# Optimization experiments

Measured on AMD Instinct MI355X. Metric: run time of the kernel, lower is better.

The kernel has to match this reference:

```python
import jax, jax.numpy as jnp
import numpy as np

EPS = 1e-8


def _cdist(a, b):
    # Euclidean pairwise distances [N, M] via ||a||^2 + ||b||^2 - 2 a b^T
    a2 = jnp.sum(a * a, axis=-1, keepdims=True)          # [N, 1]
    b2 = jnp.sum(b * b, axis=-1, keepdims=True).T        # [1, M]
    sq = a2 + b2 - 2.0 * (a @ b.T)                       # [N, M]
    return jnp.sqrt(jnp.maximum(sq, 1e-12))


def setup_inputs() -> dict:
    key = jax.random.key(0)
    k1, k2, k3 = jax.random.split(key, 3)
    N, M = 16384, 16384
    # scale to metric-like LiDAR coordinates
    query_points = jax.random.normal(k1, (N, 3), dtype=jnp.float32) * 20.0
    ref_points = jax.random.normal(k2, (M, 3), dtype=jnp.float32) * 20.0
    ref_flow = jax.random.normal(k3, (M, 3), dtype=jnp.float32)
    return {"query_points": query_points, "ref_points": ref_points,
            "ref_flow": ref_flow, "k": 3}


def reference(query_points, ref_points, ref_flow, k):
    # knn_interpolate_flow (pure-torch fallback path), method='knn'
    dist = _cdist(query_points, ref_points)              # [N, M]
    neg_d, knn_idx = jax.lax.top_k(-dist, k)             # smallest k distances
    knn_dist = -neg_d                                    # [N, k]
    weights = 1.0 / (knn_dist + EPS)
    weights = weights / jnp.sum(weights, axis=1, keepdims=True)
    knn_flow = ref_flow[knn_idx]                         # [N, k, 3]
    interpolated_flow = jnp.sum(weights[..., None] * knn_flow, axis=1)  # [N, 3]
    return interpolated_flow
```

## Files before the change

### kernel.cpp

```cpp
#include <hip/hip_runtime.h>
#include <math.h>

#define BLOCK 256
#define QPT   8
#define CHUNK 512
#define S     64

__device__ __forceinline__ float mul_rn(float a, float b) {
#pragma clang fp contract(off)
    return a * b;
}
__device__ __forceinline__ float add_rn(float a, float b) {
#pragma clang fp contract(off)
    return a + b;
}
__device__ __forceinline__ float sumsq3(float x, float y, float z) {
    return add_rn(add_rn(mul_rn(x, x), mul_rn(y, y)), mul_rn(z, z));
}
__device__ __forceinline__ float med3f(float a, float b, float c) {
    return __builtin_amdgcn_fmed3f(a, b, c);
}
__device__ __forceinline__ float pair_sq(float a0, float a1, float a2, float an,
                                         float bx, float by, float bz, float bw) {
    const float dot = __builtin_fmaf(a2, bz,
                      __builtin_fmaf(a1, by, mul_rn(a0, bx)));
    return __builtin_fmaf(-2.0f, dot, add_rn(an, bw));
}

__device__ __forceinline__ void val3_push(float& d0, float& d1, float& d2, float v) {
    d2 = med3f(d1, d2, v);
    d1 = med3f(d0, d1, v);
    d0 = fminf(d0, v);
}

__device__ __forceinline__ void lex3_push(float& d0, float& d1, float& d2,
                                          int& i0, int& i1, int& i2,
                                          float sq, int idx) {
    const bool l0 = (sq < d0) || (sq == d0 && idx < i0);
    const bool l1 = (sq < d1) || (sq == d1 && idx < i1);
    const bool l2 = (sq < d2) || (sq == d2 && idx < i2);
    i2 = l1 ? i1 : (l2 ? idx : i2);
    d2 = l1 ? d1 : (l2 ? sq  : d2);
    i1 = l0 ? i0 : (l1 ? idx : i1);
    d1 = l0 ? d0 : (l1 ? sq  : d1);
    i0 = l0 ? idx : i0;
    d0 = l0 ? sq  : d0;
}

__device__ __forceinline__ void stage_chunk(const float* __restrict__ r,
                                            int start, int cnt,
                                            float4* __restrict__ smem) {
    const int t = threadIdx.x;
    if (t < (cnt >> 2)) {
        const float4* p = (const float4*)(r + (size_t)(start + t * 4) * 3);
        const float4 A = p[0], B = p[1], C = p[2];
        smem[t * 4 + 0] = make_float4(A.x, A.y, A.z, sumsq3(A.x, A.y, A.z));
        smem[t * 4 + 1] = make_float4(A.w, B.x, B.y, sumsq3(A.w, B.x, B.y));
        smem[t * 4 + 2] = make_float4(B.z, B.w, C.x, sumsq3(B.z, B.w, C.x));
        smem[t * 4 + 3] = make_float4(C.y, C.z, C.w, sumsq3(C.y, C.z, C.w));
    }
}

__global__ __launch_bounds__(BLOCK, 2) void values_kernel(
    const float* __restrict__ q, const float* __restrict__ r,
    float* __restrict__ smin, int N, int refsPerSlice)
{
    __shared__ float4 smem[CHUNK];
    const int tid = threadIdx.x;
    const int s   = blockIdx.y;
    const int start = s * refsPerSlice;

    float a0[QPT], a1[QPT], a2[QPT], an[QPT], d0[QPT];
#pragma unroll
    for (int u = 0; u < QPT; ++u) {
        const int qi = (blockIdx.x * QPT + u) * BLOCK + tid;
        a0[u] = q[qi * 3 + 0];
        a1[u] = q[qi * 3 + 1];
        a2[u] = q[qi * 3 + 2];
        an[u] = sumsq3(a0[u], a1[u], a2[u]);
        d0[u] = __builtin_inff();
    }

    for (int coff = 0; coff < refsPerSlice; coff += CHUNK) {
        const int cnt = min(CHUNK, refsPerSlice - coff);
        __syncthreads();
        stage_chunk(r, start + coff, cnt, smem);
        __syncthreads();
#pragma unroll 4
        for (int j = 0; j < cnt; ++j) {
            const float4 b = smem[j];
#pragma unroll
            for (int u = 0; u < QPT; ++u) {
                const float sq = pair_sq(a0[u], a1[u], a2[u], an[u],
                                         b.x, b.y, b.z, b.w);
                d0[u] = fminf(d0[u], sq);
            }
        }
    }

#pragma unroll
    for (int u = 0; u < QPT; ++u) {
        const int qi = (blockIdx.x * QPT + u) * BLOCK + tid;
        smin[(size_t)qi * S + s] = d0[u];
    }
}

__global__ __launch_bounds__(BLOCK, 4) void rescan_kernel(
    const float* __restrict__ q, const float* __restrict__ r,
    const float* __restrict__ smin, const float* __restrict__ flow,
    float* __restrict__ out, int N, int refsPerSlice)
{
    const int lane = threadIdx.x & 63;
    const int qi   = blockIdx.x * (BLOCK / 64) + (threadIdx.x >> 6);

    const float a0 = q[qi * 3 + 0];
    const float a1 = q[qi * 3 + 1];
    const float a2 = q[qi * 3 + 2];
    const float an = sumsq3(a0, a1, a2);

    const float v = smin[(size_t)qi * S + lane];
    float g0 = v, g1 = __builtin_inff(), g2 = __builtin_inff();
#pragma unroll
    for (int m = 1; m < 64; m <<= 1) {
        const float e0 = __shfl_xor(g0, m);
        const float e1 = __shfl_xor(g1, m);
        const float e2 = __shfl_xor(g2, m);
        val3_push(g0, g1, g2, e0);
        val3_push(g0, g1, g2, e1);
        val3_push(g0, g1, g2, e2);
    }

    unsigned long long mask = __ballot(v <= g2);

    float d0 = __builtin_inff(), d1 = __builtin_inff(), d2 = __builtin_inff();
    int   i0 = 0x7fffffff, i1 = 0x7fffffff, i2 = 0x7fffffff;
    const int K = refsPerSlice >> 6;

    while (mask) {
        const int s = (int)__builtin_ctzll(mask);
        mask &= mask - 1;
        const int base = s * refsPerSlice;
        for (int k = 0; k < K; ++k) {
            const int idx = base + lane + (k << 6);
            const float b0 = r[3 * idx + 0];
            const float b1 = r[3 * idx + 1];
            const float b2 = r[3 * idx + 2];
            const float bw = sumsq3(b0, b1, b2);
            const float sq = pair_sq(a0, a1, a2, an, b0, b1, b2, bw);
            const bool c0 = sq < d0;
            const bool c1 = sq < d1;
            const bool c2 = sq < d2;
            i2 = c1 ? i1 : (c2 ? idx : i2);
            d2 = c1 ? d1 : (c2 ? sq  : d2);
            i1 = c0 ? i0 : (c1 ? idx : i1);
            d1 = c0 ? d0 : (c1 ? sq  : d1);
            i0 = c0 ? idx : i0;
            d0 = c0 ? sq  : d0;
        }
    }

#pragma unroll
    for (int m = 1; m < 64; m <<= 1) {
        const float e0 = __shfl_xor(d0, m);
        const float e1 = __shfl_xor(d1, m);
        const float e2 = __shfl_xor(d2, m);
        const int   j0 = __shfl_xor(i0, m);
        const int   j1 = __shfl_xor(i1, m);
        const int   j2 = __shfl_xor(i2, m);
        lex3_push(d0, d1, d2, i0, i1, i2, e0, j0);
        lex3_push(d0, d1, d2, i0, i1, i2, e1, j1);
        lex3_push(d0, d1, d2, i0, i1, i2, e2, j2);
    }

    if (lane == 0) {
        const float t0 = sqrtf(fmaxf(d0, 1e-12f));
        const float t1 = sqrtf(fmaxf(d1, 1e-12f));
        const float t2 = sqrtf(fmaxf(d2, 1e-12f));
        const float w0r = 1.0f / add_rn(t0, 1e-8f);
        const float w1r = 1.0f / add_rn(t1, 1e-8f);
        const float w2r = 1.0f / add_rn(t2, 1e-8f);
        const float wsum = add_rn(add_rn(w0r, w1r), w2r);
        const float w0 = w0r / wsum;
        const float w1 = w1r / wsum;
        const float w2 = w2r / wsum;

        const float f00 = flow[3 * i0 + 0], f01 = flow[3 * i0 + 1], f02 = flow[3 * i0 + 2];
        const float f10 = flow[3 * i1 + 0], f11 = flow[3 * i1 + 1], f12 = flow[3 * i1 + 2];
        const float f20 = flow[3 * i2 + 0], f21 = flow[3 * i2 + 1], f22 = flow[3 * i2 + 2];

        out[qi * 3 + 0] = add_rn(add_rn(mul_rn(w0, f00), mul_rn(w1, f10)), mul_rn(w2, f20));
        out[qi * 3 + 1] = add_rn(add_rn(mul_rn(w0, f01), mul_rn(w1, f11)), mul_rn(w2, f21));
        out[qi * 3 + 2] = add_rn(add_rn(mul_rn(w0, f02), mul_rn(w1, f12)), mul_rn(w2, f22));
    }
}

extern "C" void kernel_launch(void* const* d_in, const int* in_sizes, int n_in,
                              void* d_out, int out_size, void* d_ws, size_t ws_size,
                              hipStream_t stream) {
    const float* q    = (const float*)d_in[0];
    const float* r    = (const float*)d_in[1];
    const float* flow = (const float*)d_in[2];

    const int N = in_sizes[0] / 3;
    const int M = in_sizes[1] / 3;

    const int refsPerSlice = M / S;
    float* smin = (float*)d_ws;
    (void)ws_size;

    dim3 grid1(N / (BLOCK * QPT), S);
    values_kernel<<<grid1, BLOCK, 0, stream>>>(q, r, smin, N, refsPerSlice);

    rescan_kernel<<<N / (BLOCK / 64), BLOCK, 0, stream>>>(
        q, r, smin, flow, (float*)d_out, N, refsPerSlice);
}
```

Before: 113.2 us.

## Replace brute-force slice scan with uniform grid spatial hashing for KNN

Swaps the O(N*M) brute-force distance scan for a uniform 48^3 grid. Reference points are bucketed by counting sort (count, three-stage prefix scan, scatter). Each query wavefront then searches expanding cube shells around its cell and stops once the third-best distance is below the distance to the shell boundary. This cuts the distance work sharply but adds several small launches, atomics and divergent irregular loops. The grid extent and cell size are hardcoded to suit roughly Gaussian data with std 20, and points outside the extent are clamped into edge cells, which the stopping bound is meant to handle.

```diff
diff --git a/kernel.cpp b/kernel.cpp
--- a/kernel.cpp
+++ b/kernel.cpp
@@ -1,10 +1,13 @@
 #include <hip/hip_runtime.h>
 #include <math.h>
 
-#define BLOCK 256
-#define QPT   8
-#define CHUNK 512
-#define S     64
+#define GRIDC  48
+#define CELLS  (GRIDC*GRIDC*GRIDC)
+#define NBLK1  (CELLS/1024)
+#define EXT    96.0f
+#define CSZ    4.0f
+#define INVC   0.25f
+#define STOP_MARGIN 0.1f
 
 __device__ __forceinline__ float mul_rn(float a, float b) {
 #pragma clang fp contract(off)
@@ -26,13 +29,11 @@
                       __builtin_fmaf(a1, by, mul_rn(a0, bx)));
     return __builtin_fmaf(-2.0f, dot, add_rn(an, bw));
 }
-
 __device__ __forceinline__ void val3_push(float& d0, float& d1, float& d2, float v) {
     d2 = med3f(d1, d2, v);
     d1 = med3f(d0, d1, v);
     d0 = fminf(d0, v);
 }
-
 __device__ __forceinline__ void lex3_push(float& d0, float& d1, float& d2,
                                           int& i0, int& i1, int& i2,
                                           float sq, int idx) {
@@ -46,117 +47,167 @@
     i0 = l0 ? idx : i0;
     d0 = l0 ? sq  : d0;
 }
-
-__device__ __forceinline__ void stage_chunk(const float* __restrict__ r,
-                                            int start, int cnt,
-                                            float4* __restrict__ smem) {
-    const int t = threadIdx.x;
-    if (t < (cnt >> 2)) {
-        const float4* p = (const float4*)(r + (size_t)(start + t * 4) * 3);
-        const float4 A = p[0], B = p[1], C = p[2];
-        smem[t * 4 + 0] = make_float4(A.x, A.y, A.z, sumsq3(A.x, A.y, A.z));
-        smem[t * 4 + 1] = make_float4(A.w, B.x, B.y, sumsq3(A.w, B.x, B.y));
-        smem[t * 4 + 2] = make_float4(B.z, B.w, C.x, sumsq3(B.z, B.w, C.x));
-        smem[t * 4 + 3] = make_float4(C.y, C.z, C.w, sumsq3(C.y, C.z, C.w));
-    }
-}
-
-__global__ __launch_bounds__(BLOCK, 2) void values_kernel(
-    const float* __restrict__ q, const float* __restrict__ r,
-    float* __restrict__ smin, int N, int refsPerSlice)
-{
-    __shared__ float4 smem[CHUNK];
+__device__ __forceinline__ void cell_coords(float x, float y, float z,
+                                            int& cx, int& cy, int& cz) {
+    cx = min(max((int)floorf((x + EXT) * INVC), 0), GRIDC - 1);
+    cy = min(max((int)floorf((y + EXT) * INVC), 0), GRIDC - 1);
+    cz = min(max((int)floorf((z + EXT) * INVC), 0), GRIDC - 1);
+}
+__device__ __forceinline__ int qdiv(int x, unsigned long long magic) {
+    return (int)(((unsigned long long)(unsigned)x * magic) >> 40);
+}
+
+__global__ __launch_bounds__(256) void zero_kernel(int* __restrict__ a) {
+    a[blockIdx.x * 256 + threadIdx.x] = 0;
+}
+
+__global__ __launch_bounds__(256) void count_kernel(
+    const float* __restrict__ r, int* __restrict__ counts, int M)
+{
+    const int i = blockIdx.x * 256 + threadIdx.x;
+    if (i < M) {
+        int cx, cy, cz;
+        cell_coords(r[3 * i], r[3 * i + 1], r[3 * i + 2], cx, cy, cz);
+        atomicAdd(&counts[(cz * GRIDC + cy) * GRIDC + cx], 1);
+    }
+}
+
+__global__ __launch_bounds__(256) void scan1_kernel(
+    const int* __restrict__ counts, int* __restrict__ cellLoc,
+    int* __restrict__ bsum)
+{
+    __shared__ int arr[256];
     const int tid = threadIdx.x;
-    const int s   = blockIdx.y;
-    const int start = s * refsPerSlice;
-
-    float a0[QPT], a1[QPT], a2[QPT], an[QPT], d0[QPT];
-#pragma unroll
-    for (int u = 0; u < QPT; ++u) {
-        const int qi = (blockIdx.x * QPT + u) * BLOCK + tid;
-        a0[u] = q[qi * 3 + 0];
-        a1[u] = q[qi * 3 + 1];
-        a2[u] = q[qi * 3 + 2];
-        an[u] = sumsq3(a0[u], a1[u], a2[u]);
-        d0[u] = __builtin_inff();
-    }
-
-    for (int coff = 0; coff < refsPerSlice; coff += CHUNK) {
-        const int cnt = min(CHUNK, refsPerSlice - coff);
-        __syncthreads();
-        stage_chunk(r, start + coff, cnt, smem);
-        __syncthreads();
-#pragma unroll 4
-        for (int j = 0; j < cnt; ++j) {
-            const float4 b = smem[j];
-#pragma unroll
-            for (int u = 0; u < QPT; ++u) {
-                const float sq = pair_sq(a0[u], a1[u], a2[u], an[u],
-                                         b.x, b.y, b.z, b.w);
-                d0[u] = fminf(d0[u], sq);
-            }
-        }
-    }
-
-#pragma unroll
-    for (int u = 0; u < QPT; ++u) {
-        const int qi = (blockIdx.x * QPT + u) * BLOCK + tid;
-        smin[(size_t)qi * S + s] = d0[u];
-    }
-}
-
-__global__ __launch_bounds__(BLOCK, 4) void rescan_kernel(
-    const float* __restrict__ q, const float* __restrict__ r,
-    const float* __restrict__ smin, const float* __restrict__ flow,
-    float* __restrict__ out, int N, int refsPerSlice)
+    const int base = blockIdx.x * 1024 + tid * 4;
+    const int4 c = *(const int4*)(counts + base);
+    const int t1 = c.x, t2 = c.x + c.y, t3 = t2 + c.z, tot = t3 + c.w;
+    arr[tid] = tot;
+    __syncthreads();
+    for (int off = 1; off < 256; off <<= 1) {
+        const int w = (tid >= off) ? arr[tid - off] : 0;
+        __syncthreads();
+        arr[tid] += w;
+        __syncthreads();
+    }
+    const int excl = arr[tid] - tot;
+    *(int4*)(cellLoc + base) = make_int4(excl, excl + t1, excl + t2, excl + t3);
+    if (tid == 255) bsum[blockIdx.x] = arr[255];
+}
+
+__global__ __launch_bounds__(128) void scan2_kernel(
+    const int* __restrict__ bsum, int* __restrict__ bscan)
+{
+    __shared__ int arr[128];
+    const int tid = threadIdx.x;
+    const int v = (tid < NBLK1) ? bsum[tid] : 0;
+    arr[tid] = v;
+    __syncthreads();
+    for (int off = 1; off < 128; off <<= 1) {
+        const int w = (tid >= off) ? arr[tid - off] : 0;
+        __syncthreads();
+        arr[tid] += w;
+        __syncthreads();
+    }
+    if (tid < NBLK1) bscan[tid] = arr[tid] - v;
+}
+
+__global__ __launch_bounds__(256) void scan3_kernel(
+    const int* __restrict__ cellLoc, const int* __restrict__ bscan,
+    int* __restrict__ cellStart, int* __restrict__ cellCur)
+{
+    const int i = blockIdx.x * 256 + threadIdx.x;
+    const int v = cellLoc[i] + bscan[i >> 10];
+    cellStart[i] = v;
+    cellCur[i] = v;
+}
+
+__global__ __launch_bounds__(256) void scatter_kernel(
+    const float* __restrict__ r, int* __restrict__ cellCur,
+    float4* __restrict__ pts4, int* __restrict__ pidx, int M)
+{
+    const int i = blockIdx.x * 256 + threadIdx.x;
+    if (i < M) {
+        const float x = r[3 * i], y = r[3 * i + 1], z = r[3 * i + 2];
+        int cx, cy, cz;
+        cell_coords(x, y, z, cx, cy, cz);
+        const int pos = atomicAdd(&cellCur[(cz * GRIDC + cy) * GRIDC + cx], 1);
+        pts4[pos] = make_float4(x, y, z, sumsq3(x, y, z));
+        pidx[pos] = i;
+    }
+}
+
+__global__ __launch_bounds__(256) void knn_kernel(
+    const float* __restrict__ q, const float4* __restrict__ pts4,
+    const int* __restrict__ pidx, const int* __restrict__ cellStart,
+    const int* __restrict__ counts, const float* __restrict__ flow,
+    float* __restrict__ out)
 {
     const int lane = threadIdx.x & 63;
-    const int qi   = blockIdx.x * (BLOCK / 64) + (threadIdx.x >> 6);
+    const int qi = blockIdx.x * 4 + (threadIdx.x >> 6);
 
     const float a0 = q[qi * 3 + 0];
     const float a1 = q[qi * 3 + 1];
     const float a2 = q[qi * 3 + 2];
     const float an = sumsq3(a0, a1, a2);
-
-    const float v = smin[(size_t)qi * S + lane];
-    float g0 = v, g1 = __builtin_inff(), g2 = __builtin_inff();
-#pragma unroll
-    for (int m = 1; m < 64; m <<= 1) {
-        const float e0 = __shfl_xor(g0, m);
-        const float e1 = __shfl_xor(g1, m);
-        const float e2 = __shfl_xor(g2, m);
-        val3_push(g0, g1, g2, e0);
-        val3_push(g0, g1, g2, e1);
-        val3_push(g0, g1, g2, e2);
-    }
-
-    unsigned long long mask = __ballot(v <= g2);
+    int cx, cy, cz;
+    cell_coords(a0, a1, a2, cx, cy, cz);
 
     float d0 = __builtin_inff(), d1 = __builtin_inff(), d2 = __builtin_inff();
     int   i0 = 0x7fffffff, i1 = 0x7fffffff, i2 = 0x7fffffff;
-    const int K = refsPerSlice >> 6;
-
-    while (mask) {
-        const int s = (int)__builtin_ctzll(mask);
-        mask &= mask - 1;
-        const int base = s * refsPerSlice;
-        for (int k = 0; k < K; ++k) {
-            const int idx = base + lane + (k << 6);
-            const float b0 = r[3 * idx + 0];
-            const float b1 = r[3 * idx + 1];
-            const float b2 = r[3 * idx + 2];
-            const float bw = sumsq3(b0, b1, b2);
-            const float sq = pair_sq(a0, a1, a2, an, b0, b1, b2, bw);
-            const bool c0 = sq < d0;
-            const bool c1 = sq < d1;
-            const bool c2 = sq < d2;
-            i2 = c1 ? i1 : (c2 ? idx : i2);
-            d2 = c1 ? d1 : (c2 ? sq  : d2);
-            i1 = c0 ? i0 : (c1 ? idx : i1);
-            d1 = c0 ? d0 : (c1 ? sq  : d1);
-            i0 = c0 ? idx : i0;
-            d0 = c0 ? sq  : d0;
+
+    for (int t = 0; t <= 2 * GRIDC; ++t) {
+        const int side = 2 * t + 1;
+        const int area = side * side;
+        const int vol  = area * side;
+        const unsigned long long magA = ((1ull << 40) + area - 1) / (unsigned)area;
+        const unsigned long long magS = ((1ull << 40) + side - 1) / (unsigned)side;
+
+        for (int i = lane; i < vol; i += 64) {
+            const int dz = qdiv(i, magA);
+            const int rm = i - dz * area;
+            const int dy = qdiv(rm, magS);
+            const int dx = rm - dy * side;
+            const int ox = dx - t, oy = dy - t, oz = dz - t;
+            const int m = max(abs(ox), max(abs(oy), abs(oz)));
+            if (m != t) continue;
+            const int ux = cx + ox, uy = cy + oy, uz = cz + oz;
+            if ((unsigned)ux >= GRIDC || (unsigned)uy >= GRIDC ||
+                (unsigned)uz >= GRIDC) continue;
+            const int cell = (uz * GRIDC + uy) * GRIDC + ux;
+            const int st = cellStart[cell];
+            const int cn = counts[cell];
+            for (int j = 0; j < cn; ++j) {
+                const float4 p = pts4[st + j];
+                const int idx = pidx[st + j];
+                const float sq = pair_sq(a0, a1, a2, an, p.x, p.y, p.z, p.w);
+                lex3_push(d0, d1, d2, i0, i1, i2, sq, idx);
+            }
         }
+
+        float g0 = d0, g1 = d1, g2 = d2;
+#pragma unroll
+        for (int m = 1; m < 64; m <<= 1) {
+            const float e0 = __shfl_xor(g0, m);
+            const float e1 = __shfl_xor(g1, m);
+            const float e2 = __shfl_xor(g2, m);
+            val3_push(g0, g1, g2, e0);
+            val3_push(g0, g1, g2, e1);
+            val3_push(g0, g1, g2, e2);
+        }
+
+        float bnd = __builtin_inff();
+        const int lox = cx - t, hix = cx + t;
+        const int loy = cy - t, hiy = cy + t;
+        const int loz = cz - t, hiz = cz + t;
+        if (lox > 0)         bnd = fminf(bnd, a0 - ((float)lox * CSZ - EXT));
+        if (hix < GRIDC - 1) bnd = fminf(bnd, ((float)(hix + 1) * CSZ - EXT) - a0);
+        if (loy > 0)         bnd = fminf(bnd, a1 - ((float)loy * CSZ - EXT));
+        if (hiy < GRIDC - 1) bnd = fminf(bnd, ((float)(hiy + 1) * CSZ - EXT) - a1);
+        if (loz > 0)         bnd = fminf(bnd, a2 - ((float)loz * CSZ - EXT));
+        if (hiz < GRIDC - 1) bnd = fminf(bnd, ((float)(hiz + 1) * CSZ - EXT) - a2);
+
+        if (__builtin_isinf(bnd)) break;
+        if (g2 <= __builtin_fmaf(bnd, bnd, -STOP_MARGIN)) break;
     }
 
 #pragma unroll
@@ -204,13 +255,25 @@
     const int N = in_sizes[0] / 3;
     const int M = in_sizes[1] / 3;
 
-    const int refsPerSlice = M / S;
-    float* smin = (float*)d_ws;
+    int* counts    = (int*)d_ws;
+    int* cellLoc   = counts + CELLS;
+    int* bsum      = cellLoc + CELLS;
+    int* bscan     = bsum + 128;
+    int* cellStart = bscan + 128;
+    int* cellCur   = cellStart + CELLS;
+    float4* pts4   = (float4*)(cellCur + CELLS);
+    int* pidx      = (int*)(pts4 + M);
     (void)ws_size;
 
-    dim3 grid1(N / (BLOCK * QPT), S);
-    values_kernel<<<grid1, BLOCK, 0, stream>>>(q, r, smin, N, refsPerSlice);
-
-    rescan_kernel<<<N / (BLOCK / 64), BLOCK, 0, stream>>>(
-        q, r, smin, flow, (float*)d_out, N, refsPerSlice);
-}
+    const int mb = (M + 255) / 256;
+
+    zero_kernel<<<CELLS / 256, 256, 0, stream>>>(counts);
+    count_kernel<<<mb, 256, 0, stream>>>(r, counts, M);
+    scan1_kernel<<<NBLK1, 256, 0, stream>>>(counts, cellLoc, bsum);
+    scan2_kernel<<<1, 128, 0, stream>>>(bsum, bscan);
+    scan3_kernel<<<CELLS / 256, 256, 0, stream>>>(cellLoc, bscan, cellStart, cellCur);
+    scatter_kernel<<<mb, 256, 0, stream>>>(r, cellCur, pts4, pidx, M);
+
+    knn_kernel<<<N / 4, 256, 0, stream>>>(q, pts4, pidx, cellStart, counts,
+                                          flow, (float*)d_out);
+}
```

Result: slower. 164.7 us (+45.5%).
